# Performance work log

Hardware: AMD Instinct MI355X
Metric: run time of the kernel (lower is better)

## Reference

```python
import jax, jax.numpy as jnp
import numpy as np
from jax import lax

CHANNEL_N = 16
HIDDEN = 128
FIRE_RATE = 0.5
ANGLE = 0.0
B, H, W = 32, 128, 128


def _sobel_kernels(C):
    # torch code convolves over axes (W, H) of x.transpose(1,3); an NHWC conv
    # over (H, W) is equivalent if we transpose each 3x3 kernel.
    dx = np.outer([1, 2, 1], [-1, 0, 1]) / 8.0
    dy = dx.T
    c = np.cos(ANGLE * np.pi / 180)
    s = np.sin(ANGLE * np.pi / 180)
    w1 = c * dx - s * dy
    w2 = s * dx + c * dy
    k1 = jnp.tile(jnp.asarray(w1.T, jnp.float32).reshape(3, 3, 1, 1), (1, 1, 1, C))
    k2 = jnp.tile(jnp.asarray(w2.T, jnp.float32).reshape(3, 3, 1, 1), (1, 1, 1, C))
    return k1, k2  # HWIO, depthwise


def _depthwise(x, k):
    return lax.conv_general_dilated(
        x, k, window_strides=(1, 1), padding='SAME',
        dimension_numbers=('NHWC', 'HWIO', 'NHWC'),
        feature_group_count=x.shape[-1])


def _alive(x):
    # 3x3 max-pool (stride 1, SAME) on alpha channel (index 3) > 0.1
    pooled = lax.reduce_window(x[..., 3:4], -jnp.inf, lax.max,
                               (1, 3, 3, 1), (1, 1, 1, 1), 'SAME')
    return pooled > 0.1  # [B,H,W,1] bool


def setup_inputs() -> dict:
    key = jax.random.key(0)
    kx, k0, k1 = jax.random.split(key, 3)
    x = jax.random.uniform(kx, (B, H, W, CHANNEL_N), dtype=jnp.float32)
    W0 = jax.random.normal(k0, (HIDDEN, 3 * CHANNEL_N), dtype=jnp.float32) * 0.1
    b0 = jnp.zeros((HIDDEN,), dtype=jnp.float32)
    # NOTE: torch zero-inits fc1; we use small random weights for meaningful numerics.
    W1 = jax.random.normal(k1, (CHANNEL_N, HIDDEN), dtype=jnp.float32) * 0.1
    return {"x": x, "W0": W0, "b0": b0, "W1": W1, "steps": 4}


def reference(x, W0, b0, W1, steps):
    C = x.shape[-1]
    k1, k2 = _sobel_kernels(C)
    base_key = jax.random.key(42)
    for step in range(steps):
        pre_life = _alive(x)
        # perceive: identity + two depthwise Sobel convs, concat on channels
        y = jnp.concatenate([x, _depthwise(x, k1), _depthwise(x, k2)], axis=-1)  # [B,H,W,3C]
        h = jax.nn.relu(jnp.einsum('bhwc,oc->bhwo', y, W0) + b0)  # [B,H,W,HIDDEN]
        dx = jnp.einsum('bhwo,co->bhwc', h, W1)  # [B,H,W,C]
        skey = jax.random.fold_in(base_key, step)
        stoch = (jax.random.uniform(skey, (x.shape[0], x.shape[1], x.shape[2], 1))
                 < FIRE_RATE).astype(x.dtype)
        x = x + dx * stoch
        post_life = _alive(x)
        life = (pre_life & post_life).astype(x.dtype)  # [B,H,W,1]
        x = x * life
        update_grid = ((stoch * life) > 0)[..., 0]  # [B,H,W] bool (unused: get_update_grid=False)
    return x
```

## Files before the change

kernel.cpp:

```cpp
#include <hip/hip_runtime.h>

#define CHN 16
#define HID 128
#define NB 32
#define NH 128
#define NW 128
#define NPIX (NB*NH*NW)
#define TPB 256
#define HW2 66
#define HH2 6
#define WSTR 56

typedef __attribute__((ext_vector_type(8))) short bf16x8;
typedef __attribute__((ext_vector_type(4))) float f32x4;
typedef __attribute__((ext_vector_type(4))) int i32x4;

__host__ __device__ inline void threefry2x32(unsigned k0, unsigned k1,
                                             unsigned x0, unsigned x1,
                                             unsigned &o0, unsigned &o1) {
  unsigned ks2 = 0x1BD11BDAu ^ k0 ^ k1;
  unsigned v0 = x0 + k0, v1 = x1 + k1;
#define TF_R(r) { v0 += v1; v1 = (v1 << (r)) | (v1 >> (32-(r))); v1 ^= v0; }
  TF_R(13) TF_R(15) TF_R(26) TF_R(6)
  v0 += k1;  v1 += ks2 + 1u;
  TF_R(17) TF_R(29) TF_R(16) TF_R(24)
  v0 += ks2; v1 += k0 + 2u;
  TF_R(13) TF_R(15) TF_R(26) TF_R(6)
  v0 += k0;  v1 += k1 + 3u;
  TF_R(17) TF_R(29) TF_R(16) TF_R(24)
  v0 += k1;  v1 += ks2 + 4u;
  TF_R(13) TF_R(15) TF_R(26) TF_R(6)
  v0 += ks2; v1 += k0 + 5u;
#undef TF_R
  o0 = v0; o1 = v1;
}

__device__ inline unsigned short f2bf(float f) {
  return __builtin_bit_cast(unsigned short, (__bf16)f);
}
__device__ inline unsigned pk2(float lo, float hi) {
  return (unsigned)f2bf(lo) | ((unsigned)f2bf(hi) << 16);
}
__device__ inline bf16x8 cvt8(float4 a, float4 b) {
  i32x4 r;
  r[0] = (int)pk2(a.x, a.y); r[1] = (int)pk2(a.z, a.w);
  r[2] = (int)pk2(b.x, b.y); r[3] = (int)pk2(b.z, b.w);
  return __builtin_bit_cast(bf16x8, r);
}
__device__ inline float bflo(int u) {
  return __builtin_bit_cast(float, (unsigned)u << 16);
}
__device__ inline float bfhi(int u) {
  return __builtin_bit_cast(float, (unsigned)u & 0xFFFF0000u);
}

__global__ __launch_bounds__(TPB, 2) void ca_step_a(
    const float* __restrict__ xin,
    const float* __restrict__ W0g,
    const float* __restrict__ b0g,
    const float* __restrict__ W1g,
    float* __restrict__ xmid,
    float* __restrict__ alphaOut,
    unsigned char* __restrict__ preLife,
    unsigned sk0, unsigned sk1)
{
  __shared__ __align__(16) short xT[HH2 * HW2 * CHN];
  __shared__ float aT[HH2 * HW2];
  __shared__ __align__(16) short W0s[128 * WSTR];

  const int tid = threadIdx.x;
  const int w = tid >> 6, l = tid & 63;
  const int lc = l & 15, lg = l >> 4;

  const int bb = blockIdx.x >> 6;
  const int t6 = blockIdx.x & 63;
  const int R0 = (t6 >> 1) << 2;
  const int C0 = (t6 & 1) << 6;

  {
    const int o = tid >> 1;
    if ((tid & 1) == 0) {
#pragma unroll
      for (int k = 0; k < 24; k += 2)
        *(unsigned*)&W0s[o * WSTR + k] = pk2(W0g[o * 48 + k], W0g[o * 48 + k + 1]);
    } else {
#pragma unroll
      for (int k = 24; k < 48; k += 2)
        *(unsigned*)&W0s[o * WSTR + k] = pk2(W0g[o * 48 + k], W0g[o * 48 + k + 1]);
      *(unsigned*)&W0s[o * WSTR + 48] = (unsigned)f2bf(b0g[o]);
      *(unsigned*)&W0s[o * WSTR + 50] = 0u;
      *(unsigned*)&W0s[o * WSTR + 52] = 0u;
      *(unsigned*)&W0s[o * WSTR + 54] = 0u;
    }
  }

  for (int h = tid; h < HH2 * HW2; h += TPB) {
    const int r = h / HW2, c = h - r * HW2;
    const int R = R0 + r - 1, C = C0 + c - 1;
    float4 v0, v1, v2, v3;
    float av;
    if ((unsigned)R < NH && (unsigned)C < NW) {
      const float* s = xin + (((size_t)bb * NH + R) * NW + C) * CHN;
      v0 = *(const float4*)(s);
      v1 = *(const float4*)(s + 4);
      v2 = *(const float4*)(s + 8);
      v3 = *(const float4*)(s + 12);
      av = v0.w;
    } else {
      v0 = v1 = v2 = v3 = (float4){0.f, 0.f, 0.f, 0.f};
      av = -1e30f;
    }
    i32x4 u;
    u[0] = (int)pk2(v0.x, v0.y); u[1] = (int)pk2(v0.z, v0.w);
    u[2] = (int)pk2(v1.x, v1.y); u[3] = (int)pk2(v1.z, v1.w);
    *(i32x4*)&xT[h * CHN] = u;
    u[0] = (int)pk2(v2.x, v2.y); u[1] = (int)pk2(v2.z, v2.w);
    u[2] = (int)pk2(v3.x, v3.y); u[3] = (int)pk2(v3.z, v3.w);
    *(i32x4*)&xT[h * CHN + 8] = u;
    aT[h] = av;
  }

  const int p = (bb * NH + R0 + w) * NW + C0 + l;
  unsigned long long fmask;
  {
    unsigned b1_, b2_;
    threefry2x32(sk0, sk1, 0u, (unsigned)p, b1_, b2_);
    fmask = __ballot(((b1_ ^ b2_) & 0x80000000u) == 0u);
  }

  __syncthreads();

  {
    float am = -1e30f;
#pragma unroll
    for (int dr = 0; dr < 3; ++dr)
#pragma unroll
      for (int dc = 0; dc < 3; ++dc)
        am = fmaxf(am, aT[(w + dr) * HW2 + (l + dc)]);
    preLife[p] = (am > 0.1f) ? (unsigned char)1 : (unsigned char)0;
  }

  const bf16x8 zero8 = {};
  bf16x8 one8 = {};
  one8[0] = (short)0x3F80;
  const int choff = (lg & 1) << 3;
  const bool gH = (lg >= 2);
  const int sA = gH ? HW2 * CHN : CHN;
  const int sB = gH ? CHN : HW2 * CHN;

  bf16x8 Yf[4][2];
#pragma unroll
  for (int m = 0; m < 4; ++m) {
    const int q = (m << 4) + lc;
    const int base = ((w + 1) * HW2 + (q + 1)) * CHN + choff;
    const bf16x8 raw = *(const bf16x8*)&xT[base];
    const i32x4 M0 = *(const i32x4*)&xT[base - sA - sB];
    const i32x4 M1 = *(const i32x4*)&xT[base - sA];
    const i32x4 M2 = *(const i32x4*)&xT[base - sA + sB];
    const i32x4 P0 = *(const i32x4*)&xT[base + sA - sB];
    const i32x4 P1 = *(const i32x4*)&xT[base + sA];
    const i32x4 P2 = *(const i32x4*)&xT[base + sA + sB];
    i32x4 res;
#pragma unroll
    for (int k = 0; k < 4; ++k) {
      const float pl = fmaf(2.f, bflo(P1[k]), bflo(P0[k])) + bflo(P2[k]);
      const float ml = fmaf(2.f, bflo(M1[k]), bflo(M0[k])) + bflo(M2[k]);
      const float ph = fmaf(2.f, bfhi(P1[k]), bfhi(P0[k])) + bfhi(P2[k]);
      const float mh = fmaf(2.f, bfhi(M1[k]), bfhi(M0[k])) + bfhi(M2[k]);
      res[k] = (int)pk2((pl - ml) * 0.125f, (ph - mh) * 0.125f);
    }
    const bf16x8 st = __builtin_bit_cast(bf16x8, res);
    Yf[m][0] = gH ? st : raw;
    Yf[m][1] = gH ? ((lg == 2) ? one8 : zero8) : st;
  }

  bf16x8 W1f[4];
#pragma unroll
  for (int kt = 0; kt < 4; ++kt) {
    const float* src = &W1g[lc * HID + kt * 32 + (lg << 3)];
    W1f[kt] = cvt8(*(const float4*)(src), *(const float4*)(src + 4));
  }

  f32x4 dxacc[4];
#pragma unroll
  for (int m = 0; m < 4; ++m) dxacc[m] = (f32x4){0.f, 0.f, 0.f, 0.f};

#pragma unroll
  for (int kt_o = 0; kt_o < 4; ++kt_o) {
    bf16x8 Wf0[2], Wf1[2];
#pragma unroll
    for (int th = 0; th < 2; ++th) {
      const int row = ((((kt_o << 1) + th) << 4) + lc) * WSTR;
      Wf0[th] = *(const bf16x8*)&W0s[row + (lg << 3)];
      Wf1[th] = (lg < 3) ? *(const bf16x8*)&W0s[row + 32 + (lg << 3)] : zero8;
    }
#pragma unroll
    for (int m = 0; m < 4; ++m) {
      f32x4 a0 = __builtin_amdgcn_mfma_f32_16x16x32_bf16(
          Wf0[0], Yf[m][0], (f32x4){0.f, 0.f, 0.f, 0.f}, 0, 0, 0);
      a0 = __builtin_amdgcn_mfma_f32_16x16x32_bf16(Wf1[0], Yf[m][1], a0, 0, 0, 0);
      f32x4 a1 = __builtin_amdgcn_mfma_f32_16x16x32_bf16(
          Wf0[1], Yf[m][0], (f32x4){0.f, 0.f, 0.f, 0.f}, 0, 0, 0);
      a1 = __builtin_amdgcn_mfma_f32_16x16x32_bf16(Wf1[1], Yf[m][1], a1, 0, 0, 0);
      unsigned xa = pk2(fmaxf(a0[0], 0.f), fmaxf(a0[1], 0.f));
      unsigned xb = pk2(fmaxf(a0[2], 0.f), fmaxf(a0[3], 0.f));
      unsigned ya = pk2(fmaxf(a1[0], 0.f), fmaxf(a1[1], 0.f));
      unsigned yb = pk2(fmaxf(a1[2], 0.f), fmaxf(a1[3], 0.f));
      asm("v_permlane32_swap_b32 %0, %1" : "+v"(xa), "+v"(ya));
      asm("v_permlane32_swap_b32 %0, %1" : "+v"(xb), "+v"(yb));
      asm("v_permlane16_swap_b32 %0, %1" : "+v"(xa), "+v"(ya));
      asm("v_permlane16_swap_b32 %0, %1" : "+v"(xb), "+v"(yb));
      i32x4 bfr;
      bfr[0] = (int)xa; bfr[1] = (int)xb; bfr[2] = (int)ya; bfr[3] = (int)yb;
      dxacc[m] = __builtin_amdgcn_mfma_f32_16x16x32_bf16(
          W1f[kt_o], __builtin_bit_cast(bf16x8, bfr), dxacc[m], 0, 0, 0);
    }
  }

#pragma unroll
  for (int m = 0; m < 4; ++m) {
    const int q = (m << 4) + lc;
    const int P = (bb * NH + R0 + w) * NW + C0 + q;
    const float f = (float)((fmask >> q) & 1ull);
    const float* src = &xin[(size_t)P * CHN + (lg << 2)];
    float4 xc = *(const float4*)src;
    float4 xm;
    xm.x = fmaf(dxacc[m][0], f, xc.x);
    xm.y = fmaf(dxacc[m][1], f, xc.y);
    xm.z = fmaf(dxacc[m][2], f, xc.z);
    xm.w = fmaf(dxacc[m][3], f, xc.w);
    *(float4*)&xmid[(size_t)P * CHN + (lg << 2)] = xm;
    if (lg == 0) alphaOut[P] = xm.w;
  }
}

__global__ __launch_bounds__(TPB) void ca_step_b(
    const float* __restrict__ xmid,
    const float* __restrict__ alphaIn,
    const unsigned char* __restrict__ preLife,
    float* __restrict__ xout)
{
  const int p = blockIdx.x * TPB + threadIdx.x;
  const int j = p & (NW - 1);
  const int i = (p >> 7) & (NH - 1);
  float pmax = -1e30f;
#pragma unroll
  for (int dh = 0; dh < 3; ++dh) {
#pragma unroll
    for (int dw = 0; dw < 3; ++dw) {
      const int ii = i + dh - 1, jj = j + dw - 1;
      if ((unsigned)ii < NH && (unsigned)jj < NW)
        pmax = fmaxf(pmax, alphaIn[p + (dh - 1) * NW + (dw - 1)]);
    }
  }
  const float m = ((pmax > 0.1f) && (preLife[p] != 0)) ? 1.f : 0.f;
  const float* src = xmid + (size_t)p * CHN;
  float4 a = *(const float4*)(src);
  float4 b = *(const float4*)(src + 4);
  float4 c = *(const float4*)(src + 8);
  float4 d = *(const float4*)(src + 12);
  a.x *= m; a.y *= m; a.z *= m; a.w *= m;
  b.x *= m; b.y *= m; b.z *= m; b.w *= m;
  c.x *= m; c.y *= m; c.z *= m; c.w *= m;
  d.x *= m; d.y *= m; d.z *= m; d.w *= m;
  float* dst = xout + (size_t)p * CHN;
  *(float4*)(dst)      = a;
  *(float4*)(dst + 4)  = b;
  *(float4*)(dst + 8)  = c;
  *(float4*)(dst + 12) = d;
}

extern "C" void kernel_launch(void* const* d_in, const int* in_sizes, int n_in,
                              void* d_out, int out_size, void* d_ws, size_t ws_size,
                              hipStream_t stream) {
  const float* x  = (const float*)d_in[0];
  const float* W0 = (const float*)d_in[1];
  const float* b0 = (const float*)d_in[2];
  const float* W1 = (const float*)d_in[3];
  float* out = (float*)d_out;

  char* ws = (char*)d_ws;
  float* X = (float*)ws;
  float* alphaB = (float*)(ws + (size_t)NPIX * CHN * 4);
  unsigned char* pl = (unsigned char*)(ws + (size_t)NPIX * CHN * 4 + (size_t)NPIX * 4);

  const dim3 grid(NPIX / TPB), block(TPB);
  const int STEPS = 4;
  for (int s = 0; s < STEPS; ++s) {
    unsigned k0, k1;
    threefry2x32(0u, 42u, 0u, (unsigned)s, k0, k1);
    const float* src = (s == 0) ? x : X;
    ca_step_a<<<grid, block, 0, stream>>>(src, W0, b0, W1, out, alphaB, pl, k0, k1);
    float* dst = (s == STEPS - 1) ? out : X;
    ca_step_b<<<grid, block, 0, stream>>>(out, alphaB, pl, dst);
  }
}
```

Measured before the change: 213.5 us.

## Fuse life-mask pass of each step into the next step's update kernel

The post-life masking of step s moves into the step s+1 update kernel. The kernel recomputes the alpha max-pool from a 2-pixel halo and applies the life mask while loading its tile. This cuts the launches from 8 to 5 and removes the separate full read/write of the state between steps, plus the alpha side buffer. In exchange each block does redundant halo mask work and extra scattered alpha loads, and ping-pongs the prelife buffers.

Result: faster. 193.0 us (-9.6%).

```diff
diff --git a/kernel.cpp b/kernel.cpp
--- a/kernel.cpp
+++ b/kernel.cpp
@@ -9,6 +9,8 @@
 #define TPB 256
 #define HW2 66
 #define HH2 6
+#define AW2 68
+#define AH2 8
 #define WSTR 56
 
 typedef __attribute__((ext_vector_type(8))) short bf16x8;
@@ -54,20 +56,18 @@
   return __builtin_bit_cast(float, (unsigned)u & 0xFFFF0000u);
 }
 
-__global__ __launch_bounds__(TPB, 2) void ca_step_a(
-    const float* __restrict__ xin,
+template <int STAGE_MASK>
+__device__ __forceinline__ void ca_core(
+    const float* __restrict__ xprev,
+    const unsigned char* __restrict__ plIn,
     const float* __restrict__ W0g,
     const float* __restrict__ b0g,
     const float* __restrict__ W1g,
     float* __restrict__ xmid,
-    float* __restrict__ alphaOut,
-    unsigned char* __restrict__ preLife,
-    unsigned sk0, unsigned sk1)
+    unsigned char* __restrict__ plOut,
+    unsigned sk0, unsigned sk1,
+    short* W0s, short* xT, float* aT, float* aT2, unsigned char* lifeB)
 {
-  __shared__ __align__(16) short xT[HH2 * HW2 * CHN];
-  __shared__ float aT[HH2 * HW2];
-  __shared__ __align__(16) short W0s[128 * WSTR];
-
   const int tid = threadIdx.x;
   const int w = tid >> 6, l = tid & 63;
   const int lc = l & 15, lg = l >> 4;
@@ -94,17 +94,45 @@
     }
   }
 
+  if (STAGE_MASK) {
+    for (int h2 = tid; h2 < AH2 * AW2; h2 += TPB) {
+      const int r2 = h2 / AW2, c2 = h2 - r2 * AW2;
+      const int Rg = R0 + r2 - 2, Cg = C0 + c2 - 2;
+      aT2[h2] = ((unsigned)Rg < NH && (unsigned)Cg < NW)
+          ? xprev[(((size_t)bb * NH + Rg) * NW + Cg) * CHN + 3] : -1e30f;
+    }
+    __syncthreads();
+  }
+
   for (int h = tid; h < HH2 * HW2; h += TPB) {
     const int r = h / HW2, c = h - r * HW2;
     const int R = R0 + r - 1, C = C0 + c - 1;
     float4 v0, v1, v2, v3;
     float av;
+    unsigned char lf = 0;
     if ((unsigned)R < NH && (unsigned)C < NW) {
-      const float* s = xin + (((size_t)bb * NH + R) * NW + C) * CHN;
+      const size_t P = ((size_t)bb * NH + R) * NW + C;
+      const float* s = xprev + P * CHN;
       v0 = *(const float4*)(s);
       v1 = *(const float4*)(s + 4);
       v2 = *(const float4*)(s + 8);
       v3 = *(const float4*)(s + 12);
+      if (STAGE_MASK) {
+        float pool = -1e30f;
+#pragma unroll
+        for (int dr = 0; dr < 3; ++dr)
+#pragma unroll
+          for (int dc = 0; dc < 3; ++dc)
+            pool = fmaxf(pool, aT2[(r + dr) * AW2 + (c + dc)]);
+        lf = ((plIn[P] != 0) && (pool > 0.1f)) ? (unsigned char)1 : (unsigned char)0;
+        const float m = (float)lf;
+        v0.x *= m; v0.y *= m; v0.z *= m; v0.w *= m;
+        v1.x *= m; v1.y *= m; v1.z *= m; v1.w *= m;
+        v2.x *= m; v2.y *= m; v2.z *= m; v2.w *= m;
+        v3.x *= m; v3.y *= m; v3.z *= m; v3.w *= m;
+      } else {
+        lf = 1;
+      }
       av = v0.w;
     } else {
       v0 = v1 = v2 = v3 = (float4){0.f, 0.f, 0.f, 0.f};
@@ -118,6 +146,7 @@
     u[2] = (int)pk2(v3.x, v3.y); u[3] = (int)pk2(v3.z, v3.w);
     *(i32x4*)&xT[h * CHN + 8] = u;
     aT[h] = av;
+    lifeB[h] = lf;
   }
 
   const int p = (bb * NH + R0 + w) * NW + C0 + l;
@@ -137,7 +166,7 @@
 #pragma unroll
       for (int dc = 0; dc < 3; ++dc)
         am = fmaxf(am, aT[(w + dr) * HW2 + (l + dc)]);
-    preLife[p] = (am > 0.1f) ? (unsigned char)1 : (unsigned char)0;
+    plOut[p] = (am > 0.1f) ? (unsigned char)1 : (unsigned char)0;
   }
 
   const bf16x8 zero8 = {};
@@ -163,11 +192,11 @@
     i32x4 res;
 #pragma unroll
     for (int k = 0; k < 4; ++k) {
-      const float pl = fmaf(2.f, bflo(P1[k]), bflo(P0[k])) + bflo(P2[k]);
-      const float ml = fmaf(2.f, bflo(M1[k]), bflo(M0[k])) + bflo(M2[k]);
-      const float ph = fmaf(2.f, bfhi(P1[k]), bfhi(P0[k])) + bfhi(P2[k]);
-      const float mh = fmaf(2.f, bfhi(M1[k]), bfhi(M0[k])) + bfhi(M2[k]);
-      res[k] = (int)pk2((pl - ml) * 0.125f, (ph - mh) * 0.125f);
+      const float pl_ = fmaf(2.f, bflo(P1[k]), bflo(P0[k])) + bflo(P2[k]);
+      const float ml_ = fmaf(2.f, bflo(M1[k]), bflo(M0[k])) + bflo(M2[k]);
+      const float ph_ = fmaf(2.f, bfhi(P1[k]), bfhi(P0[k])) + bfhi(P2[k]);
+      const float mh_ = fmaf(2.f, bfhi(M1[k]), bfhi(M0[k])) + bfhi(M2[k]);
+      res[k] = (int)pk2((pl_ - ml_) * 0.125f, (ph_ - mh_) * 0.125f);
     }
     const bf16x8 st = __builtin_bit_cast(bf16x8, res);
     Yf[m][0] = gH ? st : raw;
@@ -179,6 +208,17 @@
   for (int kt = 0; kt < 4; ++kt) {
     const float* src = &W1g[lc * HID + kt * 32 + (lg << 3)];
     W1f[kt] = cvt8(*(const float4*)(src), *(const float4*)(src + 4));
+  }
+
+  float4 xpre[4];
+#pragma unroll
+  for (int m = 0; m < 4; ++m) {
+    const int q = (m << 4) + lc;
+    const size_t P = ((size_t)bb * NH + R0 + w) * NW + C0 + q;
+    float4 xc = *(const float4*)&xprev[P * CHN + (lg << 2)];
+    const float ml = (float)lifeB[(w + 1) * HW2 + (q + 1)];
+    xc.x *= ml; xc.y *= ml; xc.z *= ml; xc.w *= ml;
+    xpre[m] = xc;
   }
 
   f32x4 dxacc[4];
@@ -220,24 +260,52 @@
 #pragma unroll
   for (int m = 0; m < 4; ++m) {
     const int q = (m << 4) + lc;
-    const int P = (bb * NH + R0 + w) * NW + C0 + q;
+    const size_t P = ((size_t)bb * NH + R0 + w) * NW + C0 + q;
     const float f = (float)((fmask >> q) & 1ull);
-    const float* src = &xin[(size_t)P * CHN + (lg << 2)];
-    float4 xc = *(const float4*)src;
     float4 xm;
-    xm.x = fmaf(dxacc[m][0], f, xc.x);
-    xm.y = fmaf(dxacc[m][1], f, xc.y);
-    xm.z = fmaf(dxacc[m][2], f, xc.z);
-    xm.w = fmaf(dxacc[m][3], f, xc.w);
-    *(float4*)&xmid[(size_t)P * CHN + (lg << 2)] = xm;
-    if (lg == 0) alphaOut[P] = xm.w;
-  }
+    xm.x = fmaf(dxacc[m][0], f, xpre[m].x);
+    xm.y = fmaf(dxacc[m][1], f, xpre[m].y);
+    xm.z = fmaf(dxacc[m][2], f, xpre[m].z);
+    xm.w = fmaf(dxacc[m][3], f, xpre[m].w);
+    *(float4*)&xmid[P * CHN + (lg << 2)] = xm;
+  }
+}
+
+__global__ __launch_bounds__(TPB, 2) void ca_step_a(
+    const float* __restrict__ xin,
+    const float* __restrict__ W0g, const float* __restrict__ b0g,
+    const float* __restrict__ W1g,
+    float* __restrict__ xmid, unsigned char* __restrict__ plOut,
+    unsigned sk0, unsigned sk1)
+{
+  __shared__ __align__(16) short W0s[128 * WSTR];
+  __shared__ __align__(16) short xT[HH2 * HW2 * CHN];
+  __shared__ float aT[HH2 * HW2];
+  __shared__ unsigned char lifeB[HH2 * HW2];
+  ca_core<0>(xin, nullptr, W0g, b0g, W1g, xmid, plOut, sk0, sk1,
+             W0s, xT, aT, nullptr, lifeB);
+}
+
+__global__ __launch_bounds__(TPB, 2) void ca_step_f(
+    const float* __restrict__ xprev,
+    const unsigned char* __restrict__ plIn,
+    const float* __restrict__ W0g, const float* __restrict__ b0g,
+    const float* __restrict__ W1g,
+    float* __restrict__ xmid, unsigned char* __restrict__ plOut,
+    unsigned sk0, unsigned sk1)
+{
+  __shared__ __align__(16) short W0s[128 * WSTR];
+  __shared__ __align__(16) short xT[HH2 * HW2 * CHN];
+  __shared__ float aT[HH2 * HW2];
+  __shared__ float aT2[AH2 * AW2];
+  __shared__ unsigned char lifeB[HH2 * HW2];
+  ca_core<1>(xprev, plIn, W0g, b0g, W1g, xmid, plOut, sk0, sk1,
+             W0s, xT, aT, aT2, lifeB);
 }
 
 __global__ __launch_bounds__(TPB) void ca_step_b(
     const float* __restrict__ xmid,
-    const float* __restrict__ alphaIn,
-    const unsigned char* __restrict__ preLife,
+    const unsigned char* __restrict__ plIn,
     float* __restrict__ xout)
 {
   const int p = blockIdx.x * TPB + threadIdx.x;
@@ -250,10 +318,10 @@
     for (int dw = 0; dw < 3; ++dw) {
       const int ii = i + dh - 1, jj = j + dw - 1;
       if ((unsigned)ii < NH && (unsigned)jj < NW)
-        pmax = fmaxf(pmax, alphaIn[p + (dh - 1) * NW + (dw - 1)]);
-    }
-  }
-  const float m = ((pmax > 0.1f) && (preLife[p] != 0)) ? 1.f : 0.f;
+        pmax = fmaxf(pmax, xmid[((size_t)p + (dh - 1) * NW + (dw - 1)) * CHN + 3]);
+    }
+  }
+  const float m = ((pmax > 0.1f) && (plIn[p] != 0)) ? 1.f : 0.f;
   const float* src = xmid + (size_t)p * CHN;
   float4 a = *(const float4*)(src);
   float4 b = *(const float4*)(src + 4);
@@ -281,17 +349,16 @@
 
   char* ws = (char*)d_ws;
   float* X = (float*)ws;
-  float* alphaB = (float*)(ws + (size_t)NPIX * CHN * 4);
-  unsigned char* pl = (unsigned char*)(ws + (size_t)NPIX * CHN * 4 + (size_t)NPIX * 4);
+  unsigned char* pl0 = (unsigned char*)(ws + (size_t)NPIX * CHN * 4);
+  unsigned char* pl1 = pl0 + NPIX;
 
   const dim3 grid(NPIX / TPB), block(TPB);
-  const int STEPS = 4;
-  for (int s = 0; s < STEPS; ++s) {
-    unsigned k0, k1;
-    threefry2x32(0u, 42u, 0u, (unsigned)s, k0, k1);
-    const float* src = (s == 0) ? x : X;
-    ca_step_a<<<grid, block, 0, stream>>>(src, W0, b0, W1, out, alphaB, pl, k0, k1);
-    float* dst = (s == STEPS - 1) ? out : X;
-    ca_step_b<<<grid, block, 0, stream>>>(out, alphaB, pl, dst);
-  }
-}
+  unsigned k0[4], k1[4];
+  for (int s = 0; s < 4; ++s) threefry2x32(0u, 42u, 0u, (unsigned)s, k0[s], k1[s]);
+
+  ca_step_a<<<grid, block, 0, stream>>>(x, W0, b0, W1, out, pl0, k0[0], k1[0]);
+  ca_step_f<<<grid, block, 0, stream>>>(out, pl0, W0, b0, W1, X, pl1, k0[1], k1[1]);
+  ca_step_f<<<grid, block, 0, stream>>>(X, pl1, W0, b0, W1, out, pl0, k0[2], k1[2]);
+  ca_step_f<<<grid, block, 0, stream>>>(out, pl0, W0, b0, W1, X, pl1, k0[3], k1[3]);
+  ca_step_b<<<grid, block, 0, stream>>>(X, pl1, out);
+}
```
